# Performance work log

Hardware: AMD Instinct MI355X
Metric: run time of the kernel (lower is better)

The kernel has to match this reference:

```python
import jax, jax.numpy as jnp
from jax import lax
import numpy as np

SEQ = 1024
VOCAB = 50000
EMB = 300
CAS_V, CAS_D = 8, 50
POS_V, POS_D = 48, 50
IN_DIM = EMB + CAS_D + POS_D  # 400
H = 512
T = 13  # num_classes / CRF tags


def setup_inputs() -> dict:
    key = jax.random.key(0)
    ks = jax.random.split(key, 16)
    s = lambda k, shape, sc=0.05: jax.random.normal(k, shape, dtype=jnp.float32) * sc
    return {
        "x": jax.random.randint(ks[0], (SEQ,), 0, VOCAB),
        "casing": jax.random.randint(ks[1], (SEQ,), 0, CAS_V),
        "pos": jax.random.randint(ks[2], (SEQ,), 0, POS_V),
        "h0": jnp.zeros((2, H), dtype=jnp.float32),
        "c0": jnp.zeros((2, H), dtype=jnp.float32),
        "W_emb": s(ks[3], (VOCAB, EMB)),
        "W_cas": s(ks[4], (CAS_V, CAS_D)),
        "W_pos": s(ks[5], (POS_V, POS_D)),
        "Wx_f": s(ks[6], (IN_DIM, 4 * H)),
        "Wh_f": s(ks[7], (H, 4 * H)),
        "b_f": jnp.zeros((4 * H,), dtype=jnp.float32),
        "Wx_b": s(ks[8], (IN_DIM, 4 * H)),
        "Wh_b": s(ks[9], (H, 4 * H)),
        "b_b": jnp.zeros((4 * H,), dtype=jnp.float32),
        "W_out": s(ks[10], (2 * H, T)),
        "b_out": jnp.zeros((T,), dtype=jnp.float32),
        "trans": s(ks[11], (T, T), 0.1),
        "start_trans": s(ks[12], (T,), 0.1),
        "end_trans": s(ks[13], (T,), 0.1),
    }


def _lstm_dir(feat, Wx, Wh, b, h0, c0, reverse):
    # feat: [L, IN_DIM]; precompute input projection for all steps
    pre = feat @ Wx + b  # [L, 4H]

    def step(carry, p):
        h, c = carry
        z = p + h @ Wh
        i, f, g, o = jnp.split(z, 4, axis=-1)
        c = jax.nn.sigmoid(f) * c + jax.nn.sigmoid(i) * jnp.tanh(g)
        h = jax.nn.sigmoid(o) * jnp.tanh(c)
        return (h, c), h

    _, hs = lax.scan(step, (h0, c0), pre, reverse=reverse)
    return hs  # [L, H]


def _viterbi(em, trans, start_trans, end_trans):
    # em: [L, T] emission (log) scores; max-plus DP
    score0 = start_trans + em[0]

    def fwd(score, e):
        total = score[:, None] + trans  # [T, T]: prev -> next
        best = jnp.max(total, axis=0) + e
        idx = jnp.argmax(total, axis=0)
        return best, idx

    final, hist = lax.scan(fwd, score0, em[1:])  # hist: [L-1, T]
    final = final + end_trans
    last = jnp.argmax(final)

    def back(tag, idx_row):
        return idx_row[tag], tag

    first, rest = lax.scan(back, last, hist, reverse=True)
    return jnp.concatenate([first[None], rest])  # [L] int


def reference(x, casing, pos, h0, c0, W_emb, W_cas, W_pos, Wx_f, Wh_f, b_f,
              Wx_b, Wh_b, b_b, W_out, b_out, trans, start_trans, end_trans):
    # AWD-LSTM encode (eval mode: dropout identity)
    feat = jnp.concatenate([W_emb[x], W_cas[casing], W_pos[pos]], axis=-1)  # [L, 400]
    hf = _lstm_dir(feat, Wx_f, Wh_f, b_f, h0[0], c0[0], reverse=False)
    hb = _lstm_dir(feat, Wx_b, Wh_b, b_b, h0[1], c0[1], reverse=True)
    o = jnp.concatenate([hf, hb], axis=-1) @ W_out + b_out  # [L, T]
    tag_scores = jax.nn.log_softmax(o, axis=1)
    path = _viterbi(tag_scores, trans, start_trans, end_trans)
    return tag_scores, path
```

## Files before the change

kernel.cpp:

```cpp
#include <hip/hip_runtime.h>
#include <hip/hip_bf16.h>
#include <math.h>

#define SEQ 1024
#define HID 512
#define FOURH 2048
#define IND 400
#define NT 13

#define NWG_DIR 16
#define LSTM_THREADS 1024
#define JPW 32
#define WCOLS 128
#define TAG_INVALID 0xFFFFFFFFu

__device__ __forceinline__ float bf2f(unsigned short u) {
    union { unsigned u32; float f; } v;
    v.u32 = ((unsigned)u) << 16;
    return v.f;
}

__device__ __forceinline__ unsigned short f2bf(float f) {
    union { float f; unsigned u; } v;
    v.f = f;
    unsigned u = v.u;
    unsigned rounding = 0x7FFFu + ((u >> 16) & 1u);
    u += rounding;
    return (unsigned short)(u >> 16);
}

__device__ __forceinline__ float ldf(const void* p, size_t i, int isf32) {
    return isf32 ? ((const float*)p)[i] : bf2f(((const unsigned short*)p)[i]);
}

__device__ __forceinline__ float sigm(float x) { return 1.0f / (1.0f + expf(-x)); }
__device__ __forceinline__ float satz(float z) { return fminf(fmaxf(z, -60.f), 60.f); }

__global__ __launch_bounds__(64) void detect_kernel(const unsigned short* __restrict__ w,
                                                    int* __restrict__ flag) {
    int lane = threadIdx.x;
    int cnt = 0;
    for (int i = 0; i < 4; ++i) {
        unsigned short u = w[2 * (lane * 4 + i)];
        int e = (u >> 7) & 0xFF;
        if (e >= 90 && e < 127) cnt++;
    }
#pragma unroll
    for (int off = 32; off >= 1; off >>= 1) cnt += __shfl_xor(cnt, off, 64);
    if (lane == 0) *flag = (cnt < 128) ? 1 : 0;
}

__global__ void embed_kernel(const int* __restrict__ x, const int* __restrict__ cas,
                             const int* __restrict__ pos,
                             const void* __restrict__ W_emb,
                             const void* __restrict__ W_cas,
                             const void* __restrict__ W_pos,
                             float* __restrict__ feat, const int* __restrict__ dflag) {
    const int isf32 = *dflag;
    int t = blockIdx.x;
    int xi = x[t], ci = cas[t], pi = pos[t];
    for (int e = threadIdx.x; e < IND; e += blockDim.x) {
        float v;
        if (e < 300)      v = ldf(W_emb, (size_t)xi * 300 + e, isf32);
        else if (e < 350) v = ldf(W_cas, (size_t)ci * 50 + (e - 300), isf32);
        else              v = ldf(W_pos, (size_t)pi * 50 + (e - 350), isf32);
        feat[t * IND + e] = v;
    }
}

__global__ __launch_bounds__(256) void pre_gemm_kernel(const float* __restrict__ feat,
        const void* __restrict__ Wx_f, const void* __restrict__ b_f,
        const void* __restrict__ Wx_b, const void* __restrict__ b_b,
        unsigned short* __restrict__ pre, const int* __restrict__ dflag) {
    __shared__ float ftile[16 * IND];
    const int isf32 = *dflag;
    int dir = blockIdx.z;
    const void* Wx = dir ? Wx_b : Wx_f;
    const void* bb = dir ? b_b : b_f;
    unsigned short* pre_d = pre + (size_t)dir * SEQ * FOURH;
    int r0 = blockIdx.y * 16;
    int col = blockIdx.x * 256 + threadIdx.x;

    for (int idx = threadIdx.x; idx < 16 * IND; idx += 256) {
        int r = idx / IND;
        int k = idx - r * IND;
        ftile[idx] = feat[(size_t)(r0 + r) * IND + k];
    }
    __syncthreads();

    float acc[16];
    float bias = ldf(bb, col, isf32);
#pragma unroll
    for (int r = 0; r < 16; ++r) acc[r] = bias;

    if (isf32) {
        const float* W = (const float*)Wx;
        for (int kk = 0; kk < 100; ++kk) {
            int k = kk * 4;
            float w0 = W[(size_t)(k + 0) * FOURH + col];
            float w1 = W[(size_t)(k + 1) * FOURH + col];
            float w2 = W[(size_t)(k + 2) * FOURH + col];
            float w3 = W[(size_t)(k + 3) * FOURH + col];
#pragma unroll
            for (int r = 0; r < 16; ++r) {
                float4 f = *(const float4*)&ftile[r * IND + k];
                acc[r] += f.x * w0 + f.y * w1 + f.z * w2 + f.w * w3;
            }
        }
    } else {
        const unsigned short* W = (const unsigned short*)Wx;
        for (int kk = 0; kk < 100; ++kk) {
            int k = kk * 4;
            float w0 = bf2f(W[(size_t)(k + 0) * FOURH + col]);
            float w1 = bf2f(W[(size_t)(k + 1) * FOURH + col]);
            float w2 = bf2f(W[(size_t)(k + 2) * FOURH + col]);
            float w3 = bf2f(W[(size_t)(k + 3) * FOURH + col]);
#pragma unroll
            for (int r = 0; r < 16; ++r) {
                float4 f = *(const float4*)&ftile[r * IND + k];
                acc[r] += f.x * w0 + f.y * w1 + f.z * w2 + f.w * w3;
            }
        }
    }
    for (int r = 0; r < 16; ++r) pre_d[(size_t)(r0 + r) * FOURH + col] = f2bf(acc[r]);
}

__global__ __launch_bounds__(LSTM_THREADS, 4) void lstm_kernel(
        const void* __restrict__ Wh_f, const void* __restrict__ Wh_b,
        const void* __restrict__ h0, const void* __restrict__ c0,
        const unsigned short* __restrict__ pre, float* __restrict__ hsout,
        unsigned long long* hbuf, const int* __restrict__ dflag) {
    __shared__ float hs[HID];
    __shared__ float red[8 * WCOLS];
    __shared__ float zb[WCOLS];
    __shared__ float cb[JPW];

    const int isf32 = *dflag;
    const int tid = threadIdx.x;
    const int b = blockIdx.x;
    const int dir = b & 1;
    const int g = b >> 1;
    const int j0 = g * JPW;

    const void* Wh = dir ? Wh_b : Wh_f;
    const unsigned short* pre_d = pre + (size_t)dir * SEQ * FOURH;
    float* hso = hsout + (size_t)dir * SEQ * HID;
    unsigned long long* hb_d = hbuf + dir * 2 * HID;

    const int col = tid & (WCOLS - 1);
    const int seg = tid >> 7;
    const int gcol = (col >> 5) * HID + j0 + (col & 31);

    float wreg[64];
    if (isf32) {
        const float* wp = (const float*)Wh + (size_t)(seg * 64) * FOURH + gcol;
#pragma unroll
        for (int kk = 0; kk < 64; ++kk) wreg[kk] = wp[(size_t)kk * FOURH];
    } else {
        const unsigned short* wp = (const unsigned short*)Wh + (size_t)(seg * 64) * FOURH + gcol;
#pragma unroll
        for (int kk = 0; kk < 64; ++kk) wreg[kk] = bf2f(wp[(size_t)kk * FOURH]);
    }

    if (tid < JPW) {
        cb[tid] = ldf(c0, dir * HID + j0 + tid, isf32);
        int j = j0 + tid;
        float h0v = ldf(h0, dir * HID + j, isf32);
        unsigned long long w0 = ((unsigned long long)0u << 32) | (unsigned long long)__float_as_uint(h0v);
        __hip_atomic_store(&hb_d[j], w0, __ATOMIC_RELAXED, __HIP_MEMORY_SCOPE_AGENT);
        __hip_atomic_store(&hb_d[HID + j],
                           ((unsigned long long)TAG_INVALID << 32),
                           __ATOMIC_RELAXED, __HIP_MEMORY_SCOPE_AGENT);
    }
    __syncthreads();

    unsigned short zpf = 0;
    if (tid < WCOLS) {
        int t0 = dir ? (SEQ - 1) : 0;
        zpf = pre_d[(size_t)t0 * FOURH + ((tid >> 5) * HID + j0 + (tid & 31))];
    }

    for (int s = 0; s < SEQ; ++s) {
        const int t = dir ? (SEQ - 1 - s) : s;

        if (tid < HID) {
            const unsigned long long* wp = &hb_d[(s & 1) * HID + tid];
            const unsigned expect = (unsigned)s;
            unsigned long long w;
            do {
                w = __hip_atomic_load(wp, __ATOMIC_RELAXED, __HIP_MEMORY_SCOPE_AGENT);
            } while ((unsigned)(w >> 32) != expect);
            hs[tid] = __uint_as_float((unsigned)w);
        }
        if (tid < WCOLS)
            zb[tid] = bf2f(zpf);
        __syncthreads();

        if (tid < WCOLS) {
            int tn = dir ? (SEQ - 2 - s) : (s + 1);
            if (s + 1 < SEQ)
                zpf = pre_d[(size_t)tn * FOURH + ((tid >> 5) * HID + j0 + (tid & 31))];
        }

        float a0 = 0.f, a1 = 0.f, a2 = 0.f, a3 = 0.f;
        const float4* hp = (const float4*)(hs + seg * 64);
#pragma unroll
        for (int q = 0; q < 4; ++q) {
#pragma unroll
            for (int r = 0; r < 4; ++r) {
                float4 h4 = hp[q * 4 + r];
                int base = (q * 4 + r) * 4;
                if (r == 0) a0 += h4.x * wreg[base] + h4.y * wreg[base + 1] + h4.z * wreg[base + 2] + h4.w * wreg[base + 3];
                if (r == 1) a1 += h4.x * wreg[base] + h4.y * wreg[base + 1] + h4.z * wreg[base + 2] + h4.w * wreg[base + 3];
                if (r == 2) a2 += h4.x * wreg[base] + h4.y * wreg[base + 1] + h4.z * wreg[base + 2] + h4.w * wreg[base + 3];
                if (r == 3) a3 += h4.x * wreg[base] + h4.y * wreg[base + 1] + h4.z * wreg[base + 2] + h4.w * wreg[base + 3];
            }
        }
        red[seg * WCOLS + col] = (a0 + a1) + (a2 + a3);
        __syncthreads();

        if (tid < JPW) {
            int jj = tid;
            float z[4];
#pragma unroll
            for (int gt = 0; gt < 4; ++gt) {
                int c2 = gt * JPW + jj;
                float zt = zb[c2];
#pragma unroll
                for (int s8 = 0; s8 < 8; ++s8) zt += red[s8 * WCOLS + c2];
                z[gt] = satz(zt);
            }
            float cprev = cb[jj];
            float ig = sigm(z[0]);
            float fg = sigm(z[1]);
            float gg = tanhf(z[2]);
            float og = sigm(z[3]);
            float cnew = fg * cprev + ig * gg;
            cb[jj] = cnew;
            float hnew = og * tanhf(fminf(fmaxf(cnew, -60.f), 60.f));
            int jidx = j0 + jj;
            unsigned long long w = ((unsigned long long)(unsigned)(s + 1) << 32)
                                 | (unsigned long long)__float_as_uint(hnew);
            __hip_atomic_store(&hb_d[((s + 1) & 1) * HID + jidx], w,
                               __ATOMIC_RELAXED, __HIP_MEMORY_SCOPE_AGENT);
            hso[(size_t)t * HID + jidx] = hnew;
        }
    }
}

__global__ __launch_bounds__(64) void outproj_kernel(const float* __restrict__ hsout,
        const void* __restrict__ W_out, const void* __restrict__ b_out,
        float* __restrict__ out_scores, const int* __restrict__ dflag) {
    const int isf32 = *dflag;
    int t = blockIdx.x;
    int lane = threadIdx.x;
    const float* hf = hsout + (size_t)t * HID;
    const float* hb = hsout + (size_t)SEQ * HID + (size_t)t * HID;
    float acc[NT];
#pragma unroll
    for (int j = 0; j < NT; ++j) acc[j] = 0.f;
    for (int k = lane; k < HID; k += 64) {
        float a = hf[k], b2 = hb[k];
#pragma unroll
        for (int j = 0; j < NT; ++j)
            acc[j] += a * ldf(W_out, (size_t)k * NT + j, isf32)
                    + b2 * ldf(W_out, (size_t)(HID + k) * NT + j, isf32);
    }
#pragma unroll
    for (int off = 32; off >= 1; off >>= 1) {
#pragma unroll
        for (int j = 0; j < NT; ++j) acc[j] += __shfl_xor(acc[j], off, 64);
    }
    float o[NT];
    float m = -1e30f;
#pragma unroll
    for (int j = 0; j < NT; ++j) { o[j] = acc[j] + ldf(b_out, j, isf32); m = fmaxf(m, o[j]); }
    float lse = 0.f;
#pragma unroll
    for (int j = 0; j < NT; ++j) lse += expf(o[j] - m);
    lse = m + logf(lse);
    if (lane < NT)
        out_scores[t * NT + lane] = o[lane] - lse;
}

__global__ __launch_bounds__(64) void viterbi_kernel(const float* __restrict__ em,
        const void* __restrict__ trans, const void* __restrict__ strans,
        const void* __restrict__ etrans, float* __restrict__ out_path,
        const int* __restrict__ dflag) {
    __shared__ unsigned char hist[SEQ][NT];
    const int isf32 = *dflag;
    int lane = threadIdx.x;
    int j = lane < NT ? lane : 0;
    float tr[NT];
#pragma unroll
    for (int i = 0; i < NT; ++i) tr[i] = ldf(trans, i * NT + j, isf32);
    float score = ldf(strans, j, isf32) + em[j];
    for (int t = 1; t < SEQ; ++t) {
        float pe = em[t * NT + j];
        float best = -1e30f;
        int arg = 0;
#pragma unroll
        for (int i = 0; i < NT; ++i) {
            float si = __shfl(score, i, 64);
            float cand = si + tr[i];
            if (cand > best) { best = cand; arg = i; }
        }
        if (lane < NT) hist[t][lane] = (unsigned char)arg;
        score = best + pe;
    }
    score += ldf(etrans, j, isf32);
    float bmax = -1e30f;
    int last = 0;
#pragma unroll
    for (int i = 0; i < NT; ++i) {
        float si = __shfl(score, i, 64);
        if (si > bmax) { bmax = si; last = i; }
    }
    if (lane == 0) {
        int cur = last;
        out_path[SEQ - 1] = (float)cur;
        for (int t = SEQ - 1; t >= 1; --t) {
            cur = hist[t][cur];
            out_path[t - 1] = (float)cur;
        }
    }
}

extern "C" void kernel_launch(void* const* d_in, const int* in_sizes, int n_in,
                              void* d_out, int out_size, void* d_ws, size_t ws_size,
                              hipStream_t stream) {
    const int* x      = (const int*)d_in[0];
    const int* casing = (const int*)d_in[1];
    const int* posi   = (const int*)d_in[2];
    const void* h0    = d_in[3];
    const void* c0    = d_in[4];
    const void* W_emb = d_in[5];
    const void* W_cas = d_in[6];
    const void* W_pos = d_in[7];
    const void* Wx_f  = d_in[8];
    const void* Wh_f  = d_in[9];
    const void* b_f   = d_in[10];
    const void* Wx_b  = d_in[11];
    const void* Wh_b  = d_in[12];
    const void* b_b   = d_in[13];
    const void* W_out = d_in[14];
    const void* b_out = d_in[15];
    const void* trans = d_in[16];
    const void* strans = d_in[17];
    const void* etrans = d_in[18];

    char* ws = (char*)d_ws;
    int* dflag          = (int*)(ws + 448);
    float* feat         = (float*)(ws + 512);
    unsigned short* pre = (unsigned short*)(ws + 1638912);
    float* hsout        = (float*)(ws + 10027520);
    unsigned long long* hbuf = (unsigned long long*)(ws + 14221824);

    float* out_scores = (float*)d_out;
    float* out_path   = out_scores + SEQ * NT;

    detect_kernel<<<1, 64, 0, stream>>>((const unsigned short*)W_emb, dflag);

    embed_kernel<<<SEQ, 128, 0, stream>>>(x, casing, posi, W_emb, W_cas, W_pos, feat, dflag);

    dim3 g2(8, 64, 2);
    pre_gemm_kernel<<<g2, 256, 0, stream>>>(feat, Wx_f, b_f, Wx_b, b_b, pre, dflag);

    lstm_kernel<<<2 * NWG_DIR, LSTM_THREADS, 0, stream>>>(
        Wh_f, Wh_b, h0, c0, pre, hsout, hbuf, dflag);

    outproj_kernel<<<SEQ, 64, 0, stream>>>(hsout, W_out, b_out, out_scores, dflag);

    viterbi_kernel<<<1, 64, 0, stream>>>(out_scores, trans, strans, etrans, out_path, dflag);
}
```

Baseline: 2.780 ms.

## Fuse embedding into input GEMM, split LSTM across more workgroups, fuse Viterbi tail

Fuses the embedding gather into the input-projection GEMM and grows its row tile from 16 to 32, so the feat buffer is no longer written and read back. The recurrent LSTM now runs on 32 workgroups of 512 threads per direction, each owning 16 hidden units. Cell state and gate pre-activations stay in registers, the reduction uses a gate-interleaved layout read with float4, and the activations use fast exp2/rcp intrinsics. Viterbi is folded into the output-projection kernel: the last block to finish, found with an atomic counter, runs the DP, removing one launch. The changes trade more cross-workgroup polling traffic and slightly lower activation precision for a shorter per-step critical path and fewer launches.

New measurement: 2.520 ms. -9.4%, faster.

```diff
diff --git a/kernel.cpp b/kernel.cpp
--- a/kernel.cpp
+++ b/kernel.cpp
@@ -8,10 +8,10 @@
 #define IND 400
 #define NT 13
 
-#define NWG_DIR 16
-#define LSTM_THREADS 1024
-#define JPW 32
-#define WCOLS 128
+#define NWG_DIR 32
+#define LSTM_THREADS 512
+#define JPW 16
+#define WCOLS 64
 #define TAG_INVALID 0xFFFFFFFFu
 
 __device__ __forceinline__ float bf2f(unsigned short u) {
@@ -33,11 +33,17 @@
     return isf32 ? ((const float*)p)[i] : bf2f(((const unsigned short*)p)[i]);
 }
 
-__device__ __forceinline__ float sigm(float x) { return 1.0f / (1.0f + expf(-x)); }
+__device__ __forceinline__ float fsigm(float x) {
+    return __builtin_amdgcn_rcpf(1.f + __builtin_amdgcn_exp2f(-1.44269504f * x));
+}
+__device__ __forceinline__ float ftanhf(float x) {
+    return 1.f - 2.f * __builtin_amdgcn_rcpf(__builtin_amdgcn_exp2f(2.88539008f * x) + 1.f);
+}
 __device__ __forceinline__ float satz(float z) { return fminf(fmaxf(z, -60.f), 60.f); }
 
 __global__ __launch_bounds__(64) void detect_kernel(const unsigned short* __restrict__ w,
-                                                    int* __restrict__ flag) {
+                                                    int* __restrict__ flag,
+                                                    unsigned* __restrict__ vcnt) {
     int lane = threadIdx.x;
     int cnt = 0;
     for (int i = 0; i < 4; ++i) {
@@ -48,50 +54,46 @@
 #pragma unroll
     for (int off = 32; off >= 1; off >>= 1) cnt += __shfl_xor(cnt, off, 64);
     if (lane == 0) *flag = (cnt < 128) ? 1 : 0;
-}
-
-__global__ void embed_kernel(const int* __restrict__ x, const int* __restrict__ cas,
-                             const int* __restrict__ pos,
-                             const void* __restrict__ W_emb,
-                             const void* __restrict__ W_cas,
-                             const void* __restrict__ W_pos,
-                             float* __restrict__ feat, const int* __restrict__ dflag) {
-    const int isf32 = *dflag;
-    int t = blockIdx.x;
-    int xi = x[t], ci = cas[t], pi = pos[t];
-    for (int e = threadIdx.x; e < IND; e += blockDim.x) {
-        float v;
-        if (e < 300)      v = ldf(W_emb, (size_t)xi * 300 + e, isf32);
-        else if (e < 350) v = ldf(W_cas, (size_t)ci * 50 + (e - 300), isf32);
-        else              v = ldf(W_pos, (size_t)pi * 50 + (e - 350), isf32);
-        feat[t * IND + e] = v;
-    }
-}
-
-__global__ __launch_bounds__(256) void pre_gemm_kernel(const float* __restrict__ feat,
+    if (lane == 1) *vcnt = 0;
+}
+
+__global__ __launch_bounds__(256) void pre_gemm_kernel(
+        const int* __restrict__ x, const int* __restrict__ cas, const int* __restrict__ pos,
+        const void* __restrict__ W_emb, const void* __restrict__ W_cas, const void* __restrict__ W_pos,
         const void* __restrict__ Wx_f, const void* __restrict__ b_f,
         const void* __restrict__ Wx_b, const void* __restrict__ b_b,
         unsigned short* __restrict__ pre, const int* __restrict__ dflag) {
-    __shared__ float ftile[16 * IND];
+    __shared__ float ftile[32 * IND];
+    __shared__ int idxs[96];
     const int isf32 = *dflag;
     int dir = blockIdx.z;
     const void* Wx = dir ? Wx_b : Wx_f;
     const void* bb = dir ? b_b : b_f;
     unsigned short* pre_d = pre + (size_t)dir * SEQ * FOURH;
-    int r0 = blockIdx.y * 16;
+    int r0 = blockIdx.y * 32;
     int col = blockIdx.x * 256 + threadIdx.x;
-
-    for (int idx = threadIdx.x; idx < 16 * IND; idx += 256) {
+    int tid = threadIdx.x;
+
+    if (tid < 32)       idxs[tid] = x[r0 + tid];
+    else if (tid < 64)  idxs[tid] = cas[r0 + tid - 32];
+    else if (tid < 96)  idxs[tid] = pos[r0 + tid - 64];
+    __syncthreads();
+
+    for (int idx = tid; idx < 32 * IND; idx += 256) {
         int r = idx / IND;
-        int k = idx - r * IND;
-        ftile[idx] = feat[(size_t)(r0 + r) * IND + k];
+        int e = idx - r * IND;
+        float v;
+        if (e < 300)      v = ldf(W_emb, (size_t)idxs[r] * 300 + e, isf32);
+        else if (e < 350) v = ldf(W_cas, (size_t)idxs[32 + r] * 50 + (e - 300), isf32);
+        else              v = ldf(W_pos, (size_t)idxs[64 + r] * 50 + (e - 350), isf32);
+        ftile[idx] = v;
     }
     __syncthreads();
 
-    float acc[16];
+    float acc[32];
     float bias = ldf(bb, col, isf32);
 #pragma unroll
-    for (int r = 0; r < 16; ++r) acc[r] = bias;
+    for (int r = 0; r < 32; ++r) acc[r] = bias;
 
     if (isf32) {
         const float* W = (const float*)Wx;
@@ -102,7 +104,7 @@
             float w2 = W[(size_t)(k + 2) * FOURH + col];
             float w3 = W[(size_t)(k + 3) * FOURH + col];
 #pragma unroll
-            for (int r = 0; r < 16; ++r) {
+            for (int r = 0; r < 32; ++r) {
                 float4 f = *(const float4*)&ftile[r * IND + k];
                 acc[r] += f.x * w0 + f.y * w1 + f.z * w2 + f.w * w3;
             }
@@ -116,24 +118,22 @@
             float w2 = bf2f(W[(size_t)(k + 2) * FOURH + col]);
             float w3 = bf2f(W[(size_t)(k + 3) * FOURH + col]);
 #pragma unroll
-            for (int r = 0; r < 16; ++r) {
+            for (int r = 0; r < 32; ++r) {
                 float4 f = *(const float4*)&ftile[r * IND + k];
                 acc[r] += f.x * w0 + f.y * w1 + f.z * w2 + f.w * w3;
             }
         }
     }
-    for (int r = 0; r < 16; ++r) pre_d[(size_t)(r0 + r) * FOURH + col] = f2bf(acc[r]);
-}
-
-__global__ __launch_bounds__(LSTM_THREADS, 4) void lstm_kernel(
+    for (int r = 0; r < 32; ++r) pre_d[(size_t)(r0 + r) * FOURH + col] = f2bf(acc[r]);
+}
+
+__global__ __launch_bounds__(LSTM_THREADS, 2) void lstm_kernel(
         const void* __restrict__ Wh_f, const void* __restrict__ Wh_b,
         const void* __restrict__ h0, const void* __restrict__ c0,
         const unsigned short* __restrict__ pre, float* __restrict__ hsout,
         unsigned long long* hbuf, const int* __restrict__ dflag) {
     __shared__ float hs[HID];
     __shared__ float red[8 * WCOLS];
-    __shared__ float zb[WCOLS];
-    __shared__ float cb[JPW];
 
     const int isf32 = *dflag;
     const int tid = threadIdx.x;
@@ -147,9 +147,12 @@
     float* hso = hsout + (size_t)dir * SEQ * HID;
     unsigned long long* hb_d = hbuf + dir * 2 * HID;
 
-    const int col = tid & (WCOLS - 1);
-    const int seg = tid >> 7;
-    const int gcol = (col >> 5) * HID + j0 + (col & 31);
+    const int seg  = tid >> 6;
+    const int col  = tid & 63;
+    const int unit = col & 15;
+    const int gate = col >> 4;
+    const int gcol = gate * HID + j0 + unit;
+    const int redoff = seg * WCOLS + unit * 4 + gate;
 
     float wreg[64];
     if (isf32) {
@@ -162,28 +165,29 @@
         for (int kk = 0; kk < 64; ++kk) wreg[kk] = bf2f(wp[(size_t)kk * FOURH]);
     }
 
+    float creg = 0.f;
+    unsigned short zn0 = 0, zn1 = 0, zn2 = 0, zn3 = 0;
     if (tid < JPW) {
-        cb[tid] = ldf(c0, dir * HID + j0 + tid, isf32);
-        int j = j0 + tid;
-        float h0v = ldf(h0, dir * HID + j, isf32);
-        unsigned long long w0 = ((unsigned long long)0u << 32) | (unsigned long long)__float_as_uint(h0v);
-        __hip_atomic_store(&hb_d[j], w0, __ATOMIC_RELAXED, __HIP_MEMORY_SCOPE_AGENT);
-        __hip_atomic_store(&hb_d[HID + j],
+        creg = ldf(c0, dir * HID + j0 + tid, isf32);
+        float h0v = ldf(h0, dir * HID + j0 + tid, isf32);
+        __hip_atomic_store(&hb_d[j0 + tid],
+                           (unsigned long long)__float_as_uint(h0v),
+                           __ATOMIC_RELAXED, __HIP_MEMORY_SCOPE_AGENT);
+        __hip_atomic_store(&hb_d[HID + j0 + tid],
                            ((unsigned long long)TAG_INVALID << 32),
                            __ATOMIC_RELAXED, __HIP_MEMORY_SCOPE_AGENT);
+        int t0 = dir ? (SEQ - 1) : 0;
+        zn0 = pre_d[(size_t)t0 * FOURH + 0 * HID + j0 + tid];
+        zn1 = pre_d[(size_t)t0 * FOURH + 1 * HID + j0 + tid];
+        zn2 = pre_d[(size_t)t0 * FOURH + 2 * HID + j0 + tid];
+        zn3 = pre_d[(size_t)t0 * FOURH + 3 * HID + j0 + tid];
     }
     __syncthreads();
-
-    unsigned short zpf = 0;
-    if (tid < WCOLS) {
-        int t0 = dir ? (SEQ - 1) : 0;
-        zpf = pre_d[(size_t)t0 * FOURH + ((tid >> 5) * HID + j0 + (tid & 31))];
-    }
 
     for (int s = 0; s < SEQ; ++s) {
         const int t = dir ? (SEQ - 1 - s) : s;
 
-        if (tid < HID) {
+        {
             const unsigned long long* wp = &hb_d[(s & 1) * HID + tid];
             const unsigned expect = (unsigned)s;
             unsigned long long w;
@@ -192,65 +196,66 @@
             } while ((unsigned)(w >> 32) != expect);
             hs[tid] = __uint_as_float((unsigned)w);
         }
-        if (tid < WCOLS)
-            zb[tid] = bf2f(zpf);
+
+        float zc0 = 0.f, zc1 = 0.f, zc2 = 0.f, zc3 = 0.f;
+        if (tid < JPW) {
+            zc0 = bf2f(zn0); zc1 = bf2f(zn1); zc2 = bf2f(zn2); zc3 = bf2f(zn3);
+            if (s + 1 < SEQ) {
+                int tn = dir ? (SEQ - 2 - s) : (s + 1);
+                zn0 = pre_d[(size_t)tn * FOURH + 0 * HID + j0 + tid];
+                zn1 = pre_d[(size_t)tn * FOURH + 1 * HID + j0 + tid];
+                zn2 = pre_d[(size_t)tn * FOURH + 2 * HID + j0 + tid];
+                zn3 = pre_d[(size_t)tn * FOURH + 3 * HID + j0 + tid];
+            }
+        }
         __syncthreads();
-
-        if (tid < WCOLS) {
-            int tn = dir ? (SEQ - 2 - s) : (s + 1);
-            if (s + 1 < SEQ)
-                zpf = pre_d[(size_t)tn * FOURH + ((tid >> 5) * HID + j0 + (tid & 31))];
-        }
 
         float a0 = 0.f, a1 = 0.f, a2 = 0.f, a3 = 0.f;
         const float4* hp = (const float4*)(hs + seg * 64);
 #pragma unroll
-        for (int q = 0; q < 4; ++q) {
-#pragma unroll
-            for (int r = 0; r < 4; ++r) {
-                float4 h4 = hp[q * 4 + r];
-                int base = (q * 4 + r) * 4;
-                if (r == 0) a0 += h4.x * wreg[base] + h4.y * wreg[base + 1] + h4.z * wreg[base + 2] + h4.w * wreg[base + 3];
-                if (r == 1) a1 += h4.x * wreg[base] + h4.y * wreg[base + 1] + h4.z * wreg[base + 2] + h4.w * wreg[base + 3];
-                if (r == 2) a2 += h4.x * wreg[base] + h4.y * wreg[base + 1] + h4.z * wreg[base + 2] + h4.w * wreg[base + 3];
-                if (r == 3) a3 += h4.x * wreg[base] + h4.y * wreg[base + 1] + h4.z * wreg[base + 2] + h4.w * wreg[base + 3];
-            }
-        }
-        red[seg * WCOLS + col] = (a0 + a1) + (a2 + a3);
+        for (int q = 0; q < 16; ++q) {
+            float4 h4 = hp[q];
+            int base = q * 4;
+            if ((q & 3) == 0) a0 += h4.x * wreg[base] + h4.y * wreg[base + 1] + h4.z * wreg[base + 2] + h4.w * wreg[base + 3];
+            if ((q & 3) == 1) a1 += h4.x * wreg[base] + h4.y * wreg[base + 1] + h4.z * wreg[base + 2] + h4.w * wreg[base + 3];
+            if ((q & 3) == 2) a2 += h4.x * wreg[base] + h4.y * wreg[base + 1] + h4.z * wreg[base + 2] + h4.w * wreg[base + 3];
+            if ((q & 3) == 3) a3 += h4.x * wreg[base] + h4.y * wreg[base + 1] + h4.z * wreg[base + 2] + h4.w * wreg[base + 3];
+        }
+        red[redoff] = (a0 + a1) + (a2 + a3);
         __syncthreads();
 
         if (tid < JPW) {
             int jj = tid;
-            float z[4];
-#pragma unroll
-            for (int gt = 0; gt < 4; ++gt) {
-                int c2 = gt * JPW + jj;
-                float zt = zb[c2];
-#pragma unroll
-                for (int s8 = 0; s8 < 8; ++s8) zt += red[s8 * WCOLS + c2];
-                z[gt] = satz(zt);
+            float z0 = zc0, z1 = zc1, z2 = zc2, z3 = zc3;
+#pragma unroll
+            for (int s8 = 0; s8 < 8; ++s8) {
+                float4 r4 = *(const float4*)&red[s8 * WCOLS + jj * 4];
+                z0 += r4.x; z1 += r4.y; z2 += r4.z; z3 += r4.w;
             }
-            float cprev = cb[jj];
-            float ig = sigm(z[0]);
-            float fg = sigm(z[1]);
-            float gg = tanhf(z[2]);
-            float og = sigm(z[3]);
-            float cnew = fg * cprev + ig * gg;
-            cb[jj] = cnew;
-            float hnew = og * tanhf(fminf(fmaxf(cnew, -60.f), 60.f));
-            int jidx = j0 + jj;
+            z0 = satz(z0); z1 = satz(z1); z2 = satz(z2); z3 = satz(z3);
+            float ig = fsigm(z0);
+            float fg = fsigm(z1);
+            float gg = ftanhf(z2);
+            float og = fsigm(z3);
+            float cnew = fg * creg + ig * gg;
+            creg = cnew;
+            float hnew = og * ftanhf(satz(cnew));
             unsigned long long w = ((unsigned long long)(unsigned)(s + 1) << 32)
                                  | (unsigned long long)__float_as_uint(hnew);
-            __hip_atomic_store(&hb_d[((s + 1) & 1) * HID + jidx], w,
+            __hip_atomic_store(&hb_d[((s + 1) & 1) * HID + j0 + jj], w,
                                __ATOMIC_RELAXED, __HIP_MEMORY_SCOPE_AGENT);
-            hso[(size_t)t * HID + jidx] = hnew;
+            hso[(size_t)t * HID + j0 + jj] = hnew;
         }
     }
 }
 
 __global__ __launch_bounds__(64) void outproj_kernel(const float* __restrict__ hsout,
         const void* __restrict__ W_out, const void* __restrict__ b_out,
-        float* __restrict__ out_scores, const int* __restrict__ dflag) {
+        float* __restrict__ out_scores,
+        const void* __restrict__ trans, const void* __restrict__ strans,
+        const void* __restrict__ etrans, float* __restrict__ out_path,
+        unsigned* __restrict__ vcnt, const int* __restrict__ dflag) {
+    __shared__ unsigned char hist[SEQ][NT];
     const int isf32 = *dflag;
     int t = blockIdx.x;
     int lane = threadIdx.x;
@@ -280,23 +285,28 @@
     for (int j = 0; j < NT; ++j) lse += expf(o[j] - m);
     lse = m + logf(lse);
     if (lane < NT)
-        out_scores[t * NT + lane] = o[lane] - lse;
-}
-
-__global__ __launch_bounds__(64) void viterbi_kernel(const float* __restrict__ em,
-        const void* __restrict__ trans, const void* __restrict__ strans,
-        const void* __restrict__ etrans, float* __restrict__ out_path,
-        const int* __restrict__ dflag) {
-    __shared__ unsigned char hist[SEQ][NT];
-    const int isf32 = *dflag;
-    int lane = threadIdx.x;
+        __hip_atomic_store(&out_scores[t * NT + lane], o[lane] - lse,
+                           __ATOMIC_RELAXED, __HIP_MEMORY_SCOPE_AGENT);
+    __builtin_amdgcn_s_waitcnt(0);
+
+    unsigned old = 0;
+    if (lane == 0) old = atomicAdd(vcnt, 1u);
+    old = __shfl(old, 0, 64);
+    if (old != SEQ - 1) return;
+
+    const float* em = out_scores;
     int j = lane < NT ? lane : 0;
     float tr[NT];
 #pragma unroll
     for (int i = 0; i < NT; ++i) tr[i] = ldf(trans, i * NT + j, isf32);
-    float score = ldf(strans, j, isf32) + em[j];
-    for (int t = 1; t < SEQ; ++t) {
-        float pe = em[t * NT + j];
+    float score = ldf(strans, j, isf32)
+                + __hip_atomic_load(&em[j], __ATOMIC_RELAXED, __HIP_MEMORY_SCOPE_AGENT);
+    float pe_next = __hip_atomic_load(&em[NT + j], __ATOMIC_RELAXED, __HIP_MEMORY_SCOPE_AGENT);
+    for (int tt = 1; tt < SEQ; ++tt) {
+        float pe = pe_next;
+        if (tt + 1 < SEQ)
+            pe_next = __hip_atomic_load(&em[(tt + 1) * NT + j],
+                                        __ATOMIC_RELAXED, __HIP_MEMORY_SCOPE_AGENT);
         float best = -1e30f;
         int arg = 0;
 #pragma unroll
@@ -305,7 +315,7 @@
             float cand = si + tr[i];
             if (cand > best) { best = cand; arg = i; }
         }
-        if (lane < NT) hist[t][lane] = (unsigned char)arg;
+        if (lane < NT) hist[tt][lane] = (unsigned char)arg;
         score = best + pe;
     }
     score += ldf(etrans, j, isf32);
@@ -319,9 +329,9 @@
     if (lane == 0) {
         int cur = last;
         out_path[SEQ - 1] = (float)cur;
-        for (int t = SEQ - 1; t >= 1; --t) {
-            cur = hist[t][cur];
-            out_path[t - 1] = (float)cur;
+        for (int tt = SEQ - 1; tt >= 1; --tt) {
+            cur = hist[tt][cur];
+            out_path[tt - 1] = (float)cur;
         }
     }
 }
@@ -351,25 +361,23 @@
 
     char* ws = (char*)d_ws;
     int* dflag          = (int*)(ws + 448);
-    float* feat         = (float*)(ws + 512);
-    unsigned short* pre = (unsigned short*)(ws + 1638912);
-    float* hsout        = (float*)(ws + 10027520);
-    unsigned long long* hbuf = (unsigned long long*)(ws + 14221824);
+    unsigned* vcnt      = (unsigned*)(ws + 456);
+    unsigned short* pre = (unsigned short*)(ws + 512);
+    float* hsout        = (float*)(ws + 512 + 8388608);
+    unsigned long long* hbuf = (unsigned long long*)(ws + 512 + 8388608 + 4194304);
 
     float* out_scores = (float*)d_out;
     float* out_path   = out_scores + SEQ * NT;
 
-    detect_kernel<<<1, 64, 0, stream>>>((const unsigned short*)W_emb, dflag);
-
-    embed_kernel<<<SEQ, 128, 0, stream>>>(x, casing, posi, W_emb, W_cas, W_pos, feat, dflag);
-
-    dim3 g2(8, 64, 2);
-    pre_gemm_kernel<<<g2, 256, 0, stream>>>(feat, Wx_f, b_f, Wx_b, b_b, pre, dflag);
+    detect_kernel<<<1, 64, 0, stream>>>((const unsigned short*)W_emb, dflag, vcnt);
+
+    dim3 g2(8, 32, 2);
+    pre_gemm_kernel<<<g2, 256, 0, stream>>>(x, casing, posi, W_emb, W_cas, W_pos,
+                                            Wx_f, b_f, Wx_b, b_b, pre, dflag);
 
     lstm_kernel<<<2 * NWG_DIR, LSTM_THREADS, 0, stream>>>(
         Wh_f, Wh_b, h0, c0, pre, hsout, hbuf, dflag);
 
-    outproj_kernel<<<SEQ, 64, 0, stream>>>(hsout, W_out, b_out, out_scores, dflag);
-
-    viterbi_kernel<<<1, 64, 0, stream>>>(out_scores, trans, strans, etrans, out_path, dflag);
-}
+    outproj_kernel<<<SEQ, 64, 0, stream>>>(hsout, W_out, b_out, out_scores,
+                                           trans, strans, etrans, out_path, vcnt, dflag);
+}
```
